# Kernel optimization log

Measured on AMD Instinct MI355X. Metric: run time of the kernel, lower is better.

## Reference

```python
import jax, jax.numpy as jnp
import numpy as np

HEADS = 16
DV = 64  # value_out_channel
DK = 64  # key_out_channel == query_out_channel
DQ = 64  # query_out_channel


def setup_inputs() -> dict:
    key = jax.random.key(0)
    ks = jax.random.split(key, 7)
    B, Skv, Ekv = 4, 2048, 1024
    Sq, Eq = 2048, 1024
    x = jax.random.normal(ks[0], (B, Skv, Ekv), dtype=jnp.float32)
    y = jax.random.normal(ks[1], (B, Sq, Eq), dtype=jnp.float32)
    # Linear weights stored as [in, out] for x @ W; no bias on qkv (bias=False)
    Wv = jax.random.normal(ks[2], (Ekv, HEADS * DV), dtype=jnp.float32) * (Ekv ** -0.5)
    Wk = jax.random.normal(ks[3], (Ekv, HEADS * DK), dtype=jnp.float32) * (Ekv ** -0.5)
    Wq = jax.random.normal(ks[4], (Eq, HEADS * DQ), dtype=jnp.float32) * (Eq ** -0.5)
    Wu = jax.random.normal(ks[5], (HEADS * DV, DQ), dtype=jnp.float32) * ((HEADS * DV) ** -0.5)
    bu = jax.random.normal(ks[6], (DQ,), dtype=jnp.float32) * 0.01
    return {"x": x, "y": y, "Wv": Wv, "Wk": Wk, "Wq": Wq, "Wu": Wu, "bu": bu}


def reference(x, y, Wv, Wk, Wq, Wu, bu):
    B, Skv, Ekv = x.shape
    _, Sq, Eq = y.shape
    v = (x @ Wv).reshape(B, Skv, HEADS, DV)
    k = (x @ Wk).reshape(B, Skv, HEADS, DK)
    q = (y @ Wq).reshape(B, Sq, HEADS, DQ)
    # scaling uses INPUT embedding dims, as in the source
    q = q * (Eq ** -0.25)
    k = k * (Ekv ** -0.25)
    dot = jnp.einsum("bqhd,bkhd->bhqk", q, k)  # [B, H, Sq, Skv]
    attn = jax.nn.softmax(dot, axis=-1)
    out = jnp.einsum("bhqk,bkhd->bqhd", attn, v).reshape(B, Sq, HEADS * DV)
    return out @ Wu + bu
```

## Files before the change

### kernel.cpp

```cpp
#include <hip/hip_runtime.h>
#include <hip/hip_bf16.h>
#include <stdint.h>

typedef short s16x8 __attribute__((ext_vector_type(8)));
typedef float f32x4 __attribute__((ext_vector_type(4)));

#define MFMA16(a, b, c) __builtin_amdgcn_mfma_f32_16x16x32_bf16((a), (b), (c), 0, 0, 0)

__device__ __forceinline__ void gld16(const __bf16* g, __bf16* l) {
  __builtin_amdgcn_global_load_lds(
      (const __attribute__((address_space(1))) unsigned int*)g,
      (__attribute__((address_space(3))) unsigned int*)l, 16, 0, 0);
}

__global__ void probe_kernel(const unsigned short* __restrict__ x, int* __restrict__ flag) {
  int cnt = 0;
  for (int i = threadIdx.x; i < 1024; i += 64) {
    unsigned bits = ((unsigned)x[2 * i]) << 16;
    float f = __uint_as_float(bits);
    float a = fabsf(f);
    if (f == f && a >= 1e-4f && a <= 1e4f) cnt++;
  }
#pragma unroll
  for (int off = 32; off; off >>= 1) cnt += __shfl_down(cnt, off);
  if (threadIdx.x == 0) *flag = (cnt >= 512) ? 1 : 0;
}

__global__ void cvt2_kernel(const void* __restrict__ ia, const void* __restrict__ ib,
                            __bf16* __restrict__ oa, __bf16* __restrict__ ob,
                            int nvec, const int* __restrict__ flag) {
  const bool isbf = (*flag != 0);
  int i = blockIdx.x * blockDim.x + threadIdx.x;
  int stride = gridDim.x * blockDim.x;
  for (; i < 2 * nvec; i += stride) {
    int v = (i < nvec) ? i : i - nvec;
    const void* in = (i < nvec) ? ia : ib;
    __bf16* out = (i < nvec) ? oa : ob;
    if (isbf) {
      *(uint4*)&out[v * 8] = *(const uint4*)&((const __bf16*)in)[v * 8];
    } else {
      float4 a = *(const float4*)&((const float*)in)[v * 8];
      float4 b = *(const float4*)&((const float*)in)[v * 8 + 4];
      union { __bf16 h[8]; uint4 u; } pk;
      pk.h[0] = (__bf16)a.x; pk.h[1] = (__bf16)a.y; pk.h[2] = (__bf16)a.z; pk.h[3] = (__bf16)a.w;
      pk.h[4] = (__bf16)b.x; pk.h[5] = (__bf16)b.y; pk.h[6] = (__bf16)b.z; pk.h[7] = (__bf16)b.w;
      *(uint4*)&out[v * 8] = pk.u;
    }
  }
}

__global__ void tr_kernel(const void* __restrict__ in, __bf16* __restrict__ out,
                          int K, int N, const int* __restrict__ flag) {
  const bool isbf = (*flag != 0);
  __shared__ float tile[32][33];
  int tx = threadIdx.x & 31, ty = threadIdx.x >> 5;
  int n0 = blockIdx.x * 32, k0 = blockIdx.y * 32;
#pragma unroll
  for (int i = 0; i < 32; i += 8) {
    size_t idx = (size_t)(k0 + ty + i) * N + (n0 + tx);
    tile[ty + i][tx] = isbf ? (float)((const __bf16*)in)[idx] : ((const float*)in)[idx];
  }
  __syncthreads();
#pragma unroll
  for (int i = 0; i < 32; i += 8)
    out[(size_t)(n0 + ty + i) * K + (k0 + tx)] = (__bf16)tile[tx][ty + i];
}

__global__ void tr3_kernel(const void* __restrict__ w0, const void* __restrict__ w1,
                           const void* __restrict__ w2, __bf16* __restrict__ outbase,
                           const int* __restrict__ flag) {
  const bool isbf = (*flag != 0);
  const int z = blockIdx.z;
  const void* in = (z == 0) ? w0 : (z == 1) ? w1 : w2;
  __bf16* out = outbase + (size_t)z * 1024 * 1024;
  __shared__ float tile[32][33];
  int tx = threadIdx.x & 31, ty = threadIdx.x >> 5;
  int n0 = blockIdx.x * 32, k0 = blockIdx.y * 32;
#pragma unroll
  for (int i = 0; i < 32; i += 8) {
    size_t idx = (size_t)(k0 + ty + i) * 1024 + (n0 + tx);
    tile[ty + i][tx] = isbf ? (float)((const __bf16*)in)[idx] : ((const float*)in)[idx];
  }
  __syncthreads();
#pragma unroll
  for (int i = 0; i < 32; i += 8)
    out[(size_t)(n0 + ty + i) * 1024 + (k0 + tx)] = (__bf16)tile[tx][ty + i];
}

template <int BM, int BN, bool BIAS, bool C_WS>
__global__ void __launch_bounds__(256)
gemm_lds(const __bf16* __restrict__ A, const __bf16* __restrict__ Bt,
         void* __restrict__ Cv, const void* __restrict__ biasv,
         int M, int N, int K, float scale, const int* __restrict__ flag) {
  constexpr int BK = 32;
  __shared__ __attribute__((aligned(16))) __bf16 As[BM * BK];
  __shared__ __attribute__((aligned(16))) __bf16 Bs[BN * BK];
  constexpr int WM = BM / 2, WN = BN / 2;
  constexpr int MT = WM / 16, NT = WN / 16;

  const bool raw_bf = (*flag != 0);
  const int tid = threadIdx.x;
  const int wid = tid >> 6, lane = tid & 63;
  const int quad = lane >> 4, l16 = lane & 15;
  const int wm = (wid >> 1) * WM, wn = (wid & 1) * WN;
  const size_t m0 = (size_t)blockIdx.x * BM;
  const size_t n0 = (size_t)blockIdx.y * BN;

  f32x4 acc[MT][NT];
#pragma unroll
  for (int i = 0; i < MT; ++i)
#pragma unroll
    for (int j = 0; j < NT; ++j) acc[i][j] = (f32x4){0.f, 0.f, 0.f, 0.f};

  for (int k0 = 0; k0 < K; k0 += BK) {
#pragma unroll
    for (int i = 0; i < (BM * 4) / 256; ++i) {
      int s = i * 256 + tid, r = s >> 2, c = (s & 3) * 8;
      gld16(&A[(m0 + r) * K + k0 + c], &As[(i * 256 + (tid & 192)) * 8]);
    }
#pragma unroll
    for (int i = 0; i < (BN * 4) / 256; ++i) {
      int s = i * 256 + tid, r = s >> 2, c = (s & 3) * 8;
      gld16(&Bt[(n0 + r) * K + k0 + c], &Bs[(i * 256 + (tid & 192)) * 8]);
    }
    __syncthreads();

    s16x8 af[MT], bf[NT];
#pragma unroll
    for (int mt = 0; mt < MT; ++mt)
      af[mt] = *(const s16x8*)&As[(wm + mt * 16 + l16) * BK + quad * 8];
#pragma unroll
    for (int nt = 0; nt < NT; ++nt)
      bf[nt] = *(const s16x8*)&Bs[(wn + nt * 16 + l16) * BK + quad * 8];
#pragma unroll
    for (int mt = 0; mt < MT; ++mt)
#pragma unroll
      for (int nt = 0; nt < NT; ++nt)
        acc[mt][nt] = MFMA16(af[mt], bf[nt], acc[mt][nt]);
    __syncthreads();
  }

#pragma unroll
  for (int mt = 0; mt < MT; ++mt)
#pragma unroll
    for (int nt = 0; nt < NT; ++nt)
#pragma unroll
      for (int r = 0; r < 4; ++r) {
        size_t row = m0 + wm + mt * 16 + quad * 4 + r;
        size_t col = n0 + wn + nt * 16 + l16;
        float v = acc[mt][nt][r] * scale;
        if (BIAS)
          v += raw_bf ? (float)((const __bf16*)biasv)[col] : ((const float*)biasv)[col];
        if (C_WS || raw_bf) ((__bf16*)Cv)[row * N + col] = (__bf16)v;
        else                ((float*)Cv)[row * N + col] = v;
      }
}

__global__ void __launch_bounds__(256)
gemm_qkv(const __bf16* __restrict__ xb, const __bf16* __restrict__ yb,
         const __bf16* __restrict__ Wt,
         __bf16* __restrict__ qb, __bf16* __restrict__ kb, __bf16* __restrict__ vbT,
         float scq, float sck) {
  constexpr int BM = 128, BN = 128, BK = 32, K = 1024;
  __shared__ __attribute__((aligned(16))) __bf16 As[BM * BK];
  __shared__ __attribute__((aligned(16))) __bf16 Bs[BN * BK];

  const int tid = threadIdx.x;
  const int wid = tid >> 6, lane = tid & 63;
  const int quad = lane >> 4, l16 = lane & 15;
  const int wm = (wid >> 1) * 64, wn = (wid & 1) * 64;

  const int id = blockIdx.x;
  const int jj = id >> 3;
  const int ny = (id & 7) * 3 + (jj % 3);
  const int mb = jj / 3;
  const size_t m0 = (size_t)mb * BM;
  const size_t n0 = (size_t)ny * BN;
  const __bf16* A = (ny < 8) ? yb : xb;

  f32x4 acc[4][4];
#pragma unroll
  for (int i = 0; i < 4; ++i)
#pragma unroll
    for (int j = 0; j < 4; ++j) acc[i][j] = (f32x4){0.f, 0.f, 0.f, 0.f};

  for (int k0 = 0; k0 < K; k0 += BK) {
#pragma unroll
    for (int i = 0; i < 2; ++i) {
      int s = i * 256 + tid, r = s >> 2, c = (s & 3) * 8;
      gld16(&A[(m0 + r) * K + k0 + c], &As[(i * 256 + (tid & 192)) * 8]);
    }
#pragma unroll
    for (int i = 0; i < 2; ++i) {
      int s = i * 256 + tid, r = s >> 2, c = (s & 3) * 8;
      gld16(&Wt[(n0 + r) * K + k0 + c], &Bs[(i * 256 + (tid & 192)) * 8]);
    }
    __syncthreads();

    s16x8 af[4], bf[4];
#pragma unroll
    for (int mt = 0; mt < 4; ++mt)
      af[mt] = *(const s16x8*)&As[(wm + mt * 16 + l16) * BK + quad * 8];
#pragma unroll
    for (int nt = 0; nt < 4; ++nt)
      bf[nt] = *(const s16x8*)&Bs[(wn + nt * 16 + l16) * BK + quad * 8];
#pragma unroll
    for (int mt = 0; mt < 4; ++mt)
#pragma unroll
      for (int nt = 0; nt < 4; ++nt)
        acc[mt][nt] = MFMA16(af[mt], bf[nt], acc[mt][nt]);
    __syncthreads();
  }

  if (ny < 16) {
    const float s = (ny < 8) ? scq : sck;
    __bf16* C = (ny < 8) ? qb : kb;
    const int nl0 = (ny < 8) ? (int)n0 : (int)n0 - 1024;
#pragma unroll
    for (int mt = 0; mt < 4; ++mt)
#pragma unroll
      for (int nt = 0; nt < 4; ++nt)
#pragma unroll
        for (int r = 0; r < 4; ++r) {
          size_t row = m0 + wm + mt * 16 + quad * 4 + r;
          size_t col = (size_t)(nl0 + wn + nt * 16 + l16);
          C[row * 1024 + col] = (__bf16)(acc[mt][nt][r] * s);
        }
  } else {
    constexpr int LBS = 144;
    __bf16* bufA = As;
    __bf16* bufB = Bs;
    __bf16* mybuf = (wid & 1) ? bufB : bufA;
    const int colbase = (int)n0 - 2048;
    const int b = (int)(m0 >> 11);
    const int sq0 = (int)(m0 & 2047);
#pragma unroll
    for (int c = 0; c < 4; ++c) {
#pragma unroll
      for (int mt = 0; mt < 4; ++mt) {
        union { __bf16 h[4]; uint2 u; } pk;
#pragma unroll
        for (int r = 0; r < 4; ++r) pk.h[r] = (__bf16)acc[mt][c][r];
        *(uint2*)&mybuf[l16 * LBS + wm + mt * 16 + quad * 4] = pk.u;
      }
      __syncthreads();
      {
        const int p = tid >> 7;
        const __bf16* rb = p ? bufB : bufA;
        const int d16 = (tid >> 3) & 15;
        const int sc = tid & 7;
        const int colg = colbase + p * 64 + c * 16 + d16;
        const int hh = colg >> 6, dd = colg & 63;
        const size_t rowb = ((size_t)b * 16 + hh) * 64 + dd;
        uint4 v0 = *(const uint4*)&rb[d16 * LBS + sc * 16];
        uint4 v1 = *(const uint4*)&rb[d16 * LBS + sc * 16 + 8];
        *(uint4*)&vbT[rowb * 2048 + sq0 + sc * 16] = v0;
        *(uint4*)&vbT[rowb * 2048 + sq0 + sc * 16 + 8] = v1;
      }
      __syncthreads();
    }
  }
}

__global__ void __launch_bounds__(256)
gemm_out(const __bf16* __restrict__ A, const __bf16* __restrict__ Bt,
         void* __restrict__ Cv, const void* __restrict__ biasv,
         const int* __restrict__ flag) {
  constexpr int BK = 64, K = 1024, N = 64;
  __shared__ __attribute__((aligned(16))) __bf16 As[32 * BK];
  __shared__ __attribute__((aligned(16))) __bf16 Bs[64 * BK];

  const bool raw_bf = (*flag != 0);
  const int tid = threadIdx.x;
  const int wid = tid >> 6, lane = tid & 63;
  const int quad = lane >> 4, l16 = lane & 15;
  const int wm = (wid >> 1) * 16, wn = (wid & 1) * 32;
  const size_t m0 = (size_t)blockIdx.x * 32;

  f32x4 acc[2];
  acc[0] = (f32x4){0.f, 0.f, 0.f, 0.f};
  acc[1] = (f32x4){0.f, 0.f, 0.f, 0.f};

  for (int k0 = 0; k0 < K; k0 += BK) {
    {
      int r = tid >> 3, c = (tid & 7) * 8;
      gld16(&A[(m0 + r) * K + k0 + c], &As[(tid & 192) * 8]);
    }
#pragma unroll
    for (int i = 0; i < 2; ++i) {
      int s = i * 256 + tid, r = s >> 3, c = (s & 7) * 8;
      gld16(&Bt[r * K + k0 + c], &Bs[(i * 256 + (tid & 192)) * 8]);
    }
    __syncthreads();

#pragma unroll
    for (int kc = 0; kc < 2; ++kc) {
      s16x8 af = *(const s16x8*)&As[(wm + l16) * BK + kc * 32 + quad * 8];
#pragma unroll
      for (int nt = 0; nt < 2; ++nt) {
        s16x8 bf = *(const s16x8*)&Bs[(wn + nt * 16 + l16) * BK + kc * 32 + quad * 8];
        acc[nt] = MFMA16(af, bf, acc[nt]);
      }
    }
    __syncthreads();
  }

#pragma unroll
  for (int nt = 0; nt < 2; ++nt)
#pragma unroll
    for (int r = 0; r < 4; ++r) {
      size_t row = m0 + wm + quad * 4 + r;
      size_t col = (size_t)(wn + nt * 16 + l16);
      float v = acc[nt][r];
      v += raw_bf ? (float)((const __bf16*)biasv)[col] : ((const float*)biasv)[col];
      if (raw_bf) ((__bf16*)Cv)[row * N + col] = (__bf16)v;
      else        ((float*)Cv)[row * N + col] = v;
    }
}

template <int BM, int BN, bool BIAS, bool A_WS, bool C_WS>
__global__ void __launch_bounds__(256)
gemm_bt(const void* __restrict__ Av, const __bf16* __restrict__ Bt,
        void* __restrict__ Cv, const void* __restrict__ biasv,
        int M, int N, int K, float scale, const int* __restrict__ flag) {
  constexpr int BK = 32;
  constexpr int LDT = BK + 8;
  __shared__ __attribute__((aligned(16))) __bf16 As[BM][LDT];
  __shared__ __attribute__((aligned(16))) __bf16 Bs[BN][LDT];
  constexpr int WM = BM / 2, WN = BN / 2;
  constexpr int MT = WM / 16, NT = WN / 16;

  const bool raw_bf = (*flag != 0);
  const bool a_bf = A_WS ? true : raw_bf;

  const int tid = threadIdx.x;
  const int wid = tid >> 6, lane = tid & 63;
  const int quad = lane >> 4, l16 = lane & 15;
  const int wm = (wid >> 1) * WM, wn = (wid & 1) * WN;
  const size_t m0 = (size_t)blockIdx.x * BM;
  const size_t n0 = (size_t)blockIdx.y * BN;

  f32x4 acc[MT][NT];
#pragma unroll
  for (int i = 0; i < MT; ++i)
#pragma unroll
    for (int j = 0; j < NT; ++j) acc[i][j] = (f32x4){0.f, 0.f, 0.f, 0.f};

  for (int k0 = 0; k0 < K; k0 += BK) {
    if (a_bf) {
      const __bf16* A = (const __bf16*)Av;
#pragma unroll
      for (int i = 0; i < (BM * 4) / 256; ++i) {
        int s = i * 256 + tid, r = s >> 2, c = (s & 3) * 8;
        *(uint4*)&As[r][c] = *(const uint4*)&A[(m0 + r) * K + k0 + c];
      }
    } else {
      const float* A = (const float*)Av;
#pragma unroll
      for (int i = 0; i < (BM * 8) / 256; ++i) {
        int s = i * 256 + tid, r = s >> 3, c = (s & 7) * 4;
        float4 t = *(const float4*)&A[(m0 + r) * K + k0 + c];
        union { __bf16 h[4]; uint2 u; } cv;
        cv.h[0] = (__bf16)t.x; cv.h[1] = (__bf16)t.y;
        cv.h[2] = (__bf16)t.z; cv.h[3] = (__bf16)t.w;
        *(uint2*)&As[r][c] = cv.u;
      }
    }
#pragma unroll
    for (int i = 0; i < (BN * 4) / 256; ++i) {
      int s = i * 256 + tid, r = s >> 2, c = (s & 3) * 8;
      *(uint4*)&Bs[r][c] = *(const uint4*)&Bt[(n0 + r) * K + k0 + c];
    }
    __syncthreads();

    s16x8 af[MT], bf[NT];
#pragma unroll
    for (int mt = 0; mt < MT; ++mt)
      af[mt] = *(const s16x8*)&As[wm + mt * 16 + l16][quad * 8];
#pragma unroll
    for (int nt = 0; nt < NT; ++nt)
      bf[nt] = *(const s16x8*)&Bs[wn + nt * 16 + l16][quad * 8];
#pragma unroll
    for (int mt = 0; mt < MT; ++mt)
#pragma unroll
      for (int nt = 0; nt < NT; ++nt)
        acc[mt][nt] = MFMA16(af[mt], bf[nt], acc[mt][nt]);
    __syncthreads();
  }

#pragma unroll
  for (int mt = 0; mt < MT; ++mt)
#pragma unroll
    for (int nt = 0; nt < NT; ++nt)
#pragma unroll
      for (int r = 0; r < 4; ++r) {
        size_t row = m0 + wm + mt * 16 + quad * 4 + r;
        size_t col = n0 + wn + nt * 16 + l16;
        float v = acc[mt][nt][r] * scale;
        if (BIAS)
          v += raw_bf ? (float)((const __bf16*)biasv)[col] : ((const float*)biasv)[col];
        if (C_WS || raw_bf) ((__bf16*)Cv)[row * N + col] = (__bf16)v;
        else                ((float*)Cv)[row * N + col] = v;
      }
}

__global__ void __launch_bounds__(256, 4)
attn5_kernel(const __bf16* __restrict__ qg, const __bf16* __restrict__ kg,
             const __bf16* __restrict__ vtg, __bf16* __restrict__ og) {
  constexpr int SKV = 2048, QT = 128, KT = 64, SS = 1024, VS = 2048;
  constexpr int LDP = 72;
  __shared__ __attribute__((aligned(16))) __bf16 QP[QT * LDP];
  __shared__ __attribute__((aligned(16))) __bf16 Ks[KT * 64];
  __shared__ __attribute__((aligned(16))) __bf16 Vt[64 * KT];

  const int tid = threadIdx.x;
  const int wid = tid >> 6, lane = tid & 63;
  const int quad = lane >> 4, l16 = lane & 15;

  const int id = blockIdx.x;
  const int j = id >> 3;
  const int bh = (id & 7) * 8 + (j & 7);
  const int b = bh >> 4, h = bh & 15;
  const int q0 = (j >> 3) * QT;

  const __bf16* qb = qg + (size_t)b * 2048 * SS + h * 64;
  const __bf16* kb = kg + (size_t)b * 2048 * SS + h * 64;
  const __bf16* vtb = vtg + (size_t)bh * 64 * VS;
  __bf16* ob = og + (size_t)b * 2048 * SS + h * 64;

#pragma unroll
  for (int i = 0; i < 4; ++i) {
    int s = i * 256 + tid, r = s >> 3, slot = s & 7, c = slot ^ (r & 7);
    gld16(&qb[(size_t)(q0 + r) * SS + c * 8], &QP[(i * 256 + (tid & 192)) * 8]);
  }
  __syncthreads();

  s16x8 qf[2][2];
#pragma unroll
  for (int nt = 0; nt < 2; ++nt)
#pragma unroll
    for (int kc = 0; kc < 2; ++kc) {
      int row = wid * 32 + nt * 16 + l16;
      qf[nt][kc] = *(const s16x8*)&QP[row * 64 + (((quad + kc * 4) ^ (row & 7)) * 8)];
    }
  __syncthreads();

  int koff[4][2];
  int pwoff[2][4];
  int proff[2][2];
  int voff[2][4];
#pragma unroll
  for (int mtk = 0; mtk < 4; ++mtk)
#pragma unroll
    for (int kc = 0; kc < 2; ++kc) {
      int row = mtk * 16 + l16;
      koff[mtk][kc] = row * 64 + (((quad + kc * 4) ^ (row & 7)) * 8);
    }
#pragma unroll
  for (int ntq = 0; ntq < 2; ++ntq) {
    int row = wid * 32 + ntq * 16 + l16;
#pragma unroll
    for (int mtk = 0; mtk < 4; ++mtk)
      pwoff[ntq][mtk] = row * LDP + mtk * 16 + quad * 4;
#pragma unroll
    for (int kc = 0; kc < 2; ++kc)
      proff[ntq][kc] = row * LDP + kc * 32 + quad * 8;
  }
#pragma unroll
  for (int kc = 0; kc < 2; ++kc)
#pragma unroll
    for (int ntd = 0; ntd < 4; ++ntd) {
      int d = ntd * 16 + l16;
      voff[kc][ntd] = d * 64 + (((kc * 4 + quad) ^ (d & 7)) * 8);
    }

  float lsum[2] = {0.f, 0.f};
  f32x4 oacc[2][4];
#pragma unroll
  for (int mt = 0; mt < 2; ++mt)
#pragma unroll
    for (int nt = 0; nt < 4; ++nt) oacc[mt][nt] = (f32x4){0.f, 0.f, 0.f, 0.f};

  for (int kv = 0; kv < SKV; kv += KT) {
#pragma unroll
    for (int i = 0; i < 2; ++i) {
      int s = i * 256 + tid, r = s >> 3, slot = s & 7, c = slot ^ (r & 7);
      gld16(&kb[(size_t)(kv + r) * SS + c * 8], &Ks[(i * 256 + (tid & 192)) * 8]);
    }
#pragma unroll
    for (int i = 0; i < 2; ++i) {
      int s = i * 256 + tid, r = s >> 3, slot = s & 7, c = slot ^ (r & 7);
      gld16(&vtb[(size_t)r * VS + kv + c * 8], &Vt[(i * 256 + (tid & 192)) * 8]);
    }
    __syncthreads();

#pragma unroll
    for (int mtk = 0; mtk < 4; ++mtk) {
      s16x8 kfa[2];
#pragma unroll
      for (int kc = 0; kc < 2; ++kc)
        kfa[kc] = *(const s16x8*)&Ks[koff[mtk][kc]];
#pragma unroll
      for (int ntq = 0; ntq < 2; ++ntq) {
        f32x4 z = (f32x4){0.f, 0.f, 0.f, 0.f};
        __builtin_amdgcn_s_setprio(1);
        z = MFMA16(kfa[0], qf[ntq][0], z);
        z = MFMA16(kfa[1], qf[ntq][1], z);
        __builtin_amdgcn_s_setprio(0);
        union { __bf16 hh[4]; uint2 u; } pk;
        float p0 = __builtin_exp2f(z[0]);
        float p1 = __builtin_exp2f(z[1]);
        float p2 = __builtin_exp2f(z[2]);
        float p3 = __builtin_exp2f(z[3]);
        pk.hh[0] = (__bf16)p0; pk.hh[1] = (__bf16)p1;
        pk.hh[2] = (__bf16)p2; pk.hh[3] = (__bf16)p3;
        lsum[ntq] += (p0 + p1) + (p2 + p3);
        *(uint2*)&QP[pwoff[ntq][mtk]] = pk.u;
      }
    }

#pragma unroll
    for (int kc = 0; kc < 2; ++kc) {
      s16x8 pf[2], vf[4];
#pragma unroll
      for (int mt2 = 0; mt2 < 2; ++mt2)
        pf[mt2] = *(const s16x8*)&QP[proff[mt2][kc]];
#pragma unroll
      for (int ntd = 0; ntd < 4; ++ntd)
        vf[ntd] = *(const s16x8*)&Vt[voff[kc][ntd]];
      __builtin_amdgcn_s_setprio(1);
#pragma unroll
      for (int mt2 = 0; mt2 < 2; ++mt2)
#pragma unroll
        for (int ntd = 0; ntd < 4; ++ntd)
          oacc[mt2][ntd] = MFMA16(pf[mt2], vf[ntd], oacc[mt2][ntd]);
      __builtin_amdgcn_s_setprio(0);
    }
    __syncthreads();
  }

#pragma unroll
  for (int nt = 0; nt < 2; ++nt) {
    lsum[nt] += __shfl_xor(lsum[nt], 16);
    lsum[nt] += __shfl_xor(lsum[nt], 32);
  }
#pragma unroll
  for (int mt2 = 0; mt2 < 2; ++mt2)
#pragma unroll
    for (int r = 0; r < 4; ++r) {
      float l = __shfl(lsum[mt2], quad * 4 + r);
      float linv = 1.0f / l;
      int row = q0 + wid * 32 + mt2 * 16 + quad * 4 + r;
#pragma unroll
      for (int ntd = 0; ntd < 4; ++ntd)
        ob[(size_t)row * SS + ntd * 16 + l16] = (__bf16)(oacc[mt2][ntd][r] * linv);
    }
}

__global__ void __launch_bounds__(256)
attn_kernel(const __bf16* __restrict__ qg, const __bf16* __restrict__ kg,
            const __bf16* __restrict__ vg, __bf16* __restrict__ og) {
  constexpr int D = 64, SKV = 2048, QT = 128, KT = 64, SS = 1024;
  constexpr int LDP = 72, LDV = 72;
  __shared__ __attribute__((aligned(16))) __bf16 QP[QT * LDP];
  __shared__ __attribute__((aligned(16))) __bf16 Ks[KT * D];
  __shared__ __attribute__((aligned(16))) __bf16 Vts[D * LDV];

  const int tid = threadIdx.x;
  const int wid = tid >> 6, lane = tid & 63;
  const int quad = lane >> 4, l16 = lane & 15;
  const int b = blockIdx.y >> 4, h = blockIdx.y & 15;
  const int q0 = blockIdx.x * QT;

  const __bf16* qb = qg + (size_t)b * 2048 * SS + h * D;
  const __bf16* kb = kg + (size_t)b * 2048 * SS + h * D;
  const __bf16* vb = vg + (size_t)b * 2048 * SS + h * D;
  __bf16* ob = og + (size_t)b * 2048 * SS + h * D;

#pragma unroll
  for (int i = 0; i < 4; ++i) {
    int s = i * 256 + tid, r = s >> 3, slot = s & 7, c = slot ^ (r & 7);
    gld16(&qb[(size_t)(q0 + r) * SS + c * 8], &QP[(i * 256 + (tid & 192)) * 8]);
  }
  __syncthreads();

  s16x8 qf[2][2];
#pragma unroll
  for (int nt = 0; nt < 2; ++nt)
#pragma unroll
    for (int kc = 0; kc < 2; ++kc) {
      int row = wid * 32 + nt * 16 + l16;
      qf[nt][kc] = *(const s16x8*)&QP[row * 64 + (((quad + kc * 4) ^ (row & 7)) * 8)];
    }
  __syncthreads();

  float lsum[2] = {0.f, 0.f};
  f32x4 oacc[2][4];
#pragma unroll
  for (int mt = 0; mt < 2; ++mt)
#pragma unroll
    for (int nt = 0; nt < 4; ++nt) oacc[mt][nt] = (f32x4){0.f, 0.f, 0.f, 0.f};

  for (int kv = 0; kv < SKV; kv += KT) {
#pragma unroll
    for (int i = 0; i < 2; ++i) {
      int s = i * 256 + tid, r = s >> 3, slot = s & 7, c = slot ^ (r & 7);
      gld16(&kb[(size_t)(kv + r) * SS + c * 8], &Ks[(i * 256 + (tid & 192)) * 8]);
    }
#pragma unroll
    for (int i = 0; i < 2; ++i) {
      int s = i * 256 + tid, r = s >> 3, mc = s & 7;
      uint4 t = *(const uint4*)&vb[(size_t)(kv + r) * SS + mc * 8];
      const __bf16* tp = (const __bf16*)&t;
      int colbase = r ^ (mc << 3);
#pragma unroll
      for (int jj = 0; jj < 8; ++jj) Vts[(mc * 8 + jj) * LDV + colbase] = tp[jj];
    }
    __syncthreads();

#pragma unroll
    for (int mtk = 0; mtk < 4; ++mtk) {
      s16x8 kfa[2];
#pragma unroll
      for (int kc = 0; kc < 2; ++kc) {
        int row = mtk * 16 + l16;
        kfa[kc] = *(const s16x8*)&Ks[row * 64 + (((quad + kc * 4) ^ (row & 7)) * 8)];
      }
#pragma unroll
      for (int ntq = 0; ntq < 2; ++ntq) {
        f32x4 z = (f32x4){0.f, 0.f, 0.f, 0.f};
        z = MFMA16(kfa[0], qf[ntq][0], z);
        z = MFMA16(kfa[1], qf[ntq][1], z);
        union { __bf16 hh[4]; uint2 u; } pk;
        float ps = 0.f;
#pragma unroll
        for (int r = 0; r < 4; ++r) {
          float p = __builtin_exp2f(fminf(z[r], 80.f));
          ps += p;
          pk.hh[r] = (__bf16)p;
        }
        lsum[ntq] += ps;
        int row = wid * 32 + ntq * 16 + l16;
        *(uint2*)&QP[row * LDP + mtk * 16 + quad * 4] = pk.u;
      }
    }

#pragma unroll
    for (int kc = 0; kc < 2; ++kc) {
      s16x8 pf[2], vf[4];
#pragma unroll
      for (int mt2 = 0; mt2 < 2; ++mt2)
        pf[mt2] = *(const s16x8*)&QP[(wid * 32 + mt2 * 16 + l16) * LDP + kc * 32 + quad * 8];
#pragma unroll
      for (int ntd = 0; ntd < 4; ++ntd) {
        int d = ntd * 16 + l16;
        int col0 = (kc * 32 + quad * 8) ^ ((((d >> 3) & 7)) << 3);
        vf[ntd] = *(const s16x8*)&Vts[d * LDV + col0];
      }
#pragma unroll
      for (int mt2 = 0; mt2 < 2; ++mt2)
#pragma unroll
        for (int ntd = 0; ntd < 4; ++ntd)
          oacc[mt2][ntd] = MFMA16(pf[mt2], vf[ntd], oacc[mt2][ntd]);
    }
    __syncthreads();
  }

#pragma unroll
  for (int nt = 0; nt < 2; ++nt) {
    lsum[nt] += __shfl_xor(lsum[nt], 16);
    lsum[nt] += __shfl_xor(lsum[nt], 32);
  }
#pragma unroll
  for (int mt2 = 0; mt2 < 2; ++mt2)
#pragma unroll
    for (int r = 0; r < 4; ++r) {
      float l = __shfl(lsum[mt2], quad * 4 + r);
      float linv = 1.0f / l;
      int row = q0 + wid * 32 + mt2 * 16 + quad * 4 + r;
#pragma unroll
      for (int ntd = 0; ntd < 4; ++ntd)
        ob[(size_t)row * SS + ntd * 16 + l16] = (__bf16)(oacc[mt2][ntd][r] * linv);
    }
}

extern "C" void kernel_launch(void* const* d_in, const int* in_sizes, int n_in,
                              void* d_out, int out_size, void* d_ws, size_t ws_size,
                              hipStream_t stream) {
  const void* x  = d_in[0];
  const void* y  = d_in[1];
  const void* Wv = d_in[2];
  const void* Wk = d_in[3];
  const void* Wq = d_in[4];
  const void* Wu = d_in[5];
  const void* bu = d_in[6];

  const float sc  = 0.17677669529663687f;
  const float scq = 0.17677669529663687f * 1.4426950408889634f;

  constexpr size_t NTOK = (size_t)8192 * 1024;
  constexpr size_t TB = NTOK * 2;

  char* p = (char*)d_ws;
  int* flag = (int*)p; p += 256;
  __bf16* qb = (__bf16*)p; p += TB;
  __bf16* kb = (__bf16*)p; p += TB;
  __bf16* vb = (__bf16*)p; p += TB;
  __bf16* WuT = (__bf16*)p; p += (size_t)64 * 1024 * 2;

  probe_kernel<<<1, 64, 0, stream>>>((const unsigned short*)x, flag);

  const size_t fast_need = 256 + 3 * TB + (size_t)64 * 1024 * 2 + 2 * TB + 3 * (size_t)1024 * 1024 * 2;
  if (ws_size >= fast_need) {
    __bf16* xb = (__bf16*)p; p += TB;
    __bf16* yb = (__bf16*)p; p += TB;
    __bf16* WqkvT = (__bf16*)p;
    __bf16* vbT = vb;
    __bf16* ob  = xb;

    cvt2_kernel<<<2048, 256, 0, stream>>>(x, y, xb, yb, (int)(NTOK / 8), flag);
    tr3_kernel<<<dim3(32, 32, 3), 256, 0, stream>>>(Wq, Wk, Wv, WqkvT, flag);
    tr_kernel<<<dim3(2, 32), 256, 0, stream>>>(Wu, WuT, 1024, 64, flag);

    gemm_qkv<<<dim3(1536), 256, 0, stream>>>(xb, yb, WqkvT, qb, kb, vbT, scq, sc);

    attn5_kernel<<<dim3(1024), 256, 0, stream>>>(qb, kb, vbT, ob);

    gemm_out<<<dim3(256), 256, 0, stream>>>(ob, WuT, d_out, bu, flag);
  } else {
    __bf16* region = (__bf16*)p;
    __bf16* WqT = region;
    __bf16* WkT = region + (size_t)1024 * 1024;
    __bf16* WvT = region + (size_t)2 * 1024 * 1024;
    __bf16* ob  = region;

    tr3_kernel<<<dim3(32, 32, 3), 256, 0, stream>>>(Wq, Wk, Wv, WqT, flag);
    tr_kernel<<<dim3(2, 32), 256, 0, stream>>>(Wu, WuT, 1024, 64, flag);

    gemm_bt<128, 128, false, false, true><<<dim3(64, 8), 256, 0, stream>>>(
        y, WqT, qb, nullptr, 8192, 1024, 1024, scq, flag);
    gemm_bt<128, 128, false, false, true><<<dim3(64, 8), 256, 0, stream>>>(
        x, WkT, kb, nullptr, 8192, 1024, 1024, sc, flag);
    gemm_bt<128, 128, false, false, true><<<dim3(64, 8), 256, 0, stream>>>(
        x, WvT, vb, nullptr, 8192, 1024, 1024, 1.0f, flag);

    attn_kernel<<<dim3(16, 64), 256, 0, stream>>>(qb, kb, vb, ob);

    gemm_bt<128, 64, true, true, false><<<dim3(64, 1), 256, 0, stream>>>(
        ob, WuT, d_out, bu, 8192, 64, 1024, 1.0f, flag);
  }
}
```

Measured before the change: 307.8 us.

## Split K/V tile loads across attention phases and use raw hardware exp2

The attention loop now prefetches the next K tile into LDS during the P·V phase. The V tile is loaded while the Q·K and softmax phase runs, and the two full __syncthreads points are replaced by vmcnt waits plus barriers placed between the phases. The aim is to hide global-to-LDS latency behind MFMA work instead of stalling at the start of each tile. It also swaps __builtin_exp2f for the raw v_exp_f32 instruction, which skips the range and denormal handling the library version may add. Buffers are still single, so the overlap only holds if the barrier placement keeps the Ks, Vt and QP reuse race-free.

```diff
diff --git a/kernel.cpp b/kernel.cpp
--- a/kernel.cpp
+++ b/kernel.cpp
@@ -11,6 +11,16 @@
   __builtin_amdgcn_global_load_lds(
       (const __attribute__((address_space(1))) unsigned int*)g,
       (__attribute__((address_space(3))) unsigned int*)l, 16, 0, 0);
+}
+
+__device__ __forceinline__ float fast_exp2(float x) {
+#if __has_builtin(__builtin_amdgcn_exp2f)
+  return __builtin_amdgcn_exp2f(x);
+#else
+  float r;
+  asm("v_exp_f32 %0, %1" : "=v"(r) : "v"(x));
+  return r;
+#endif
 }
 
 __global__ void probe_kernel(const unsigned short* __restrict__ x, int* __restrict__ flag) {
@@ -481,18 +491,21 @@
 #pragma unroll
     for (int nt = 0; nt < 4; ++nt) oacc[mt][nt] = (f32x4){0.f, 0.f, 0.f, 0.f};
 
+#pragma unroll
+  for (int i = 0; i < 2; ++i) {
+    int s = i * 256 + tid, r = s >> 3, slot = s & 7, c = slot ^ (r & 7);
+    gld16(&kb[(size_t)r * SS + c * 8], &Ks[(i * 256 + (tid & 192)) * 8]);
+  }
+
   for (int kv = 0; kv < SKV; kv += KT) {
-#pragma unroll
-    for (int i = 0; i < 2; ++i) {
-      int s = i * 256 + tid, r = s >> 3, slot = s & 7, c = slot ^ (r & 7);
-      gld16(&kb[(size_t)(kv + r) * SS + c * 8], &Ks[(i * 256 + (tid & 192)) * 8]);
-    }
+    asm volatile("s_waitcnt vmcnt(0)" ::: "memory");
+    __builtin_amdgcn_s_barrier();
+
 #pragma unroll
     for (int i = 0; i < 2; ++i) {
       int s = i * 256 + tid, r = s >> 3, slot = s & 7, c = slot ^ (r & 7);
       gld16(&vtb[(size_t)r * VS + kv + c * 8], &Vt[(i * 256 + (tid & 192)) * 8]);
     }
-    __syncthreads();
 
 #pragma unroll
     for (int mtk = 0; mtk < 4; ++mtk) {
@@ -508,10 +521,10 @@
         z = MFMA16(kfa[1], qf[ntq][1], z);
         __builtin_amdgcn_s_setprio(0);
         union { __bf16 hh[4]; uint2 u; } pk;
-        float p0 = __builtin_exp2f(z[0]);
-        float p1 = __builtin_exp2f(z[1]);
-        float p2 = __builtin_exp2f(z[2]);
-        float p3 = __builtin_exp2f(z[3]);
+        float p0 = fast_exp2(z[0]);
+        float p1 = fast_exp2(z[1]);
+        float p2 = fast_exp2(z[2]);
+        float p3 = fast_exp2(z[3]);
         pk.hh[0] = (__bf16)p0; pk.hh[1] = (__bf16)p1;
         pk.hh[2] = (__bf16)p2; pk.hh[3] = (__bf16)p3;
         lsum[ntq] += (p0 + p1) + (p2 + p3);
@@ -519,6 +532,17 @@
       }
     }
 
+    asm volatile("s_waitcnt vmcnt(0)" ::: "memory");
+    __builtin_amdgcn_s_barrier();
+
+    if (kv + KT < SKV) {
+#pragma unroll
+      for (int i = 0; i < 2; ++i) {
+        int s = i * 256 + tid, r = s >> 3, slot = s & 7, c = slot ^ (r & 7);
+        gld16(&kb[(size_t)(kv + KT + r) * SS + c * 8], &Ks[(i * 256 + (tid & 192)) * 8]);
+      }
+    }
+
 #pragma unroll
     for (int kc = 0; kc < 2; ++kc) {
       s16x8 pf[2], vf[4];
@@ -536,7 +560,6 @@
           oacc[mt2][ntd] = MFMA16(pf[mt2], vf[ntd], oacc[mt2][ntd]);
       __builtin_amdgcn_s_setprio(0);
     }
-    __syncthreads();
   }
 
 #pragma unroll
```

New measurement: 278.8 us. 1.1x faster.
